# Optimization experiments

Hardware: AMD Instinct MI355X
Metric: run time of the kernel (lower is better)

The kernel has to match this reference:

```python
import jax, jax.numpy as jnp
import numpy as np

N, K, D_IN, D_OUT = 50000, 16, 256, 256
LN_EPS = 1e-5


def setup_inputs() -> dict:
    key = jax.random.key(0)
    k1, k2, k3, k4 = jax.random.split(key, 4)
    features = jax.random.normal(k1, (N, D_IN), dtype=jnp.float32)
    neighbors = jax.random.randint(k2, (N, K), 0, N, dtype=jnp.int64)
    importance_weights = jax.random.uniform(k3, (N, K), dtype=jnp.float32)
    # Linear(in_channels, out_channels): weight stored as [D_IN, D_OUT] for x @ W + b
    W = jax.random.normal(k4, (D_IN, D_OUT), dtype=jnp.float32) * (1.0 / np.sqrt(D_IN))
    b = jnp.zeros((D_OUT,), dtype=jnp.float32)
    gamma = jnp.ones((D_OUT,), dtype=jnp.float32)
    beta = jnp.zeros((D_OUT,), dtype=jnp.float32)
    return {"features": features, "neighbors": neighbors,
            "importance_weights": importance_weights,
            "W": W, "b": b, "gamma": gamma, "beta": beta}


def reference(features, neighbors, importance_weights, W, b, gamma, beta):
    # Gather neighbor features: [N, K, D_IN]
    neigh_feats = features[neighbors]
    # Linear transform: [N, K, D_OUT]
    transformed = jnp.einsum('nkd,df->nkf', neigh_feats, W) + b
    # Normalize importance weights per node; zero-sum fallback = uniform mean
    wsum = jnp.sum(importance_weights, axis=-1, keepdims=True)  # [N, 1]
    norm_w = jnp.where(wsum == 0.0,
                       jnp.full_like(importance_weights, 1.0 / K),
                       importance_weights / jnp.where(wsum == 0.0, 1.0, wsum))
    # Importance-weighted sum over neighbors: [N, D_OUT]
    agg = jnp.einsum('nkf,nk->nf', transformed, norm_w)
    # LayerNorm over feature dim (torch: biased variance, eps=1e-5)
    mean = jnp.mean(agg, axis=-1, keepdims=True)
    var = jnp.mean((agg - mean) ** 2, axis=-1, keepdims=True)
    out = (agg - mean) * jax.lax.rsqrt(var + LN_EPS) * gamma + beta
    return out
```

## Files before the change

kernel.cpp:

```cpp
#include <hip/hip_runtime.h>


#define NN   50000
#define KNB  16
#define D    256

typedef __attribute__((ext_vector_type(8))) short short8;
typedef __attribute__((ext_vector_type(4))) float f32x4;

static __device__ __forceinline__ unsigned short f2bf(float x) {
    unsigned int u = __float_as_uint(x);
    return (unsigned short)((u + 0x7FFFu + ((u >> 16) & 1u)) >> 16);
}
static __device__ __forceinline__ float bf2f(unsigned short h) {
    return __uint_as_float((unsigned int)h << 16);
}

__global__ __launch_bounds__(256) void convert_all(const float* __restrict__ feat,
                                                   const float* __restrict__ Wm,
                                                   unsigned short* __restrict__ featb,
                                                   unsigned short* __restrict__ wtp) {
    if (blockIdx.x < 6250) {
        const size_t g = (size_t)blockIdx.x * 256 + threadIdx.x;
        const float4 a = *(const float4*)(feat + g * 8);
        const float4 b = *(const float4*)(feat + g * 8 + 4);
        short8 o;
        o[0] = (short)f2bf(a.x); o[1] = (short)f2bf(a.y);
        o[2] = (short)f2bf(a.z); o[3] = (short)f2bf(a.w);
        o[4] = (short)f2bf(b.x); o[5] = (short)f2bf(b.y);
        o[6] = (short)f2bf(b.z); o[7] = (short)f2bf(b.w);
        *(short8*)(featb + g * 8) = o;
    } else {
        const int g    = (blockIdx.x - 6250) * 256 + threadIdx.x;
        const int lane = g & 63;
        const int kb   = (g >> 6) & 7;
        const int c    = g >> 9;
        const int n    = c * 16 + (lane & 15);
        const int k0   = kb * 32 + (lane >> 4) * 8;
        short8 v;
        #pragma unroll
        for (int j = 0; j < 8; ++j) v[j] = (short)f2bf(Wm[(size_t)(k0 + j) * D + n]);
        *(short8*)(wtp + (size_t)g * 8) = v;
    }
}

__global__ __launch_bounds__(256, 8) void pool_b(const unsigned short* __restrict__ featb,
                                                 const int*   __restrict__ nbr,
                                                 const float* __restrict__ iw,
                                                 unsigned short* __restrict__ aggb) {
    const int  t    = threadIdx.x;
    const int  lane = t & 63;
    const int  wq   = t >> 6;
    const long n    = (long)blockIdx.x * 4 + wq;

    float ws = 0.f;
    #pragma unroll
    for (int k = 0; k < KNB; ++k) ws += iw[n * KNB + k];
    const bool  zs  = (ws == 0.f);
    const float inv = zs ? (1.f / KNB) : (1.f / ws);

    float4 p = make_float4(0.f, 0.f, 0.f, 0.f);
    #pragma unroll 1
    for (int kb = 0; kb < KNB; kb += 8) {
        int   idx[8];
        float w[8];
        #pragma unroll
        for (int k = 0; k < 8; ++k) {
            idx[k] = nbr[n * KNB + kb + k];
            w[k]   = iw [n * KNB + kb + k];
        }
        #pragma unroll
        for (int k = 0; k < 8; ++k) {
            const float   wk = zs ? inv : (w[k] * inv);
            const ushort4 u  = *(const ushort4*)(featb + (size_t)idx[k] * D + lane * 4);
            p.x += wk * bf2f(u.x); p.y += wk * bf2f(u.y);
            p.z += wk * bf2f(u.z); p.w += wk * bf2f(u.w);
        }
    }
    ushort4 o;
    o.x = f2bf(p.x); o.y = f2bf(p.y); o.z = f2bf(p.z); o.w = f2bf(p.w);
    *(ushort4*)(aggb + (size_t)n * 512 + lane * 4) = o;
}

__global__ __launch_bounds__(256, 8) void pool_f(const float* __restrict__ feat,
                                                 const int*   __restrict__ nbr,
                                                 const float* __restrict__ iw,
                                                 unsigned short* __restrict__ aggb) {
    const int  t    = threadIdx.x;
    const int  lane = t & 63;
    const int  wq   = t >> 6;
    const long n    = (long)blockIdx.x * 4 + wq;
    float ws = 0.f;
    #pragma unroll
    for (int k = 0; k < KNB; ++k) ws += iw[n * KNB + k];
    const bool  zs  = (ws == 0.f);
    const float inv = zs ? (1.f / KNB) : (1.f / ws);
    float4 p = make_float4(0.f, 0.f, 0.f, 0.f);
    #pragma unroll 1
    for (int kb = 0; kb < KNB; kb += 8) {
        int idx[8]; float w[8];
        #pragma unroll
        for (int k = 0; k < 8; ++k) { idx[k] = nbr[n*KNB+kb+k]; w[k] = iw[n*KNB+kb+k]; }
        #pragma unroll
        for (int k = 0; k < 8; ++k) {
            const float  wk = zs ? inv : (w[k] * inv);
            const float4 f  = *(const float4*)(feat + (size_t)idx[k] * D + lane * 4);
            p.x += wk*f.x; p.y += wk*f.y; p.z += wk*f.z; p.w += wk*f.w;
        }
    }
    ushort4 o;
    o.x = f2bf(p.x); o.y = f2bf(p.y); o.z = f2bf(p.z); o.w = f2bf(p.w);
    *(ushort4*)(aggb + (size_t)n * 512 + lane * 4) = o;
}

#define WSTR 272
__global__ __launch_bounds__(256) void gemm_ln(const unsigned short* __restrict__ aggb,
                                               const unsigned short* __restrict__ wtp,
                                               const float* __restrict__ bias,
                                               const float* __restrict__ gamma,
                                               const float* __restrict__ beta,
                                               float* __restrict__ out) {
    __shared__ float fsh[4][4 * WSTR];

    const int t       = threadIdx.x;
    const int lane    = t & 63;
    const int wq      = t >> 6;
    const int quad    = lane >> 4;
    const int l15     = lane & 15;
    const int rowbase = blockIdx.x * 64 + wq * 16;

    const int arow = min(rowbase + l15, NN - 1);
    const unsigned short* aptr = aggb + (size_t)arow * 512 + quad * 8;
    const short8* wv = (const short8*)wtp;

    f32x4 acc[16];
    #pragma unroll
    for (int c = 0; c < 16; ++c) acc[c] = (f32x4){0.f, 0.f, 0.f, 0.f};

    #pragma unroll
    for (int kb = 0; kb < 8; ++kb) {
        const short8 a = *(const short8*)(aptr + kb * 32);
        #pragma unroll
        for (int c = 0; c < 16; ++c) {
            const short8 b = wv[(size_t)(c * 8 + kb) * 64 + lane];
            acc[c] = __builtin_amdgcn_mfma_f32_16x16x32_bf16(a, b, acc[c], 0, 0, 0);
        }
    }

    float bv[16];
    #pragma unroll
    for (int c = 0; c < 16; ++c) bv[c] = bias[c * 16 + l15];
    const float4 gv4 = *(const float4*)(gamma + lane * 4);
    const float4 bt4 = *(const float4*)(beta  + lane * 4);
    float* wsh = fsh[wq];

    #pragma unroll
    for (int j = 0; j < 4; ++j) {
        float s = 0.f, sq = 0.f;
        #pragma unroll
        for (int c = 0; c < 16; ++c) {
            const float v = acc[c][j] + bv[c];
            s += v; sq += v * v;
        }
        #pragma unroll
        for (int off = 1; off < 16; off <<= 1) {
            s  += __shfl_xor(s,  off, 64);
            sq += __shfl_xor(sq, off, 64);
        }
        const float mean = s * (1.f / D);
        const float var  = sq * (1.f / D) - mean * mean;
        const float rstd = rsqrtf(var + 1e-5f);
        #pragma unroll
        for (int c = 0; c < 16; ++c)
            wsh[quad * WSTR + c * 16 + l15] = (acc[c][j] + bv[c] - mean) * rstd;
        #pragma unroll
        for (int p = 0; p < 4; ++p) {
            const long  r  = rowbase + p * 4 + j;
            const float4 v = *(const float4*)(wsh + p * WSTR + lane * 4);
            float4 o;
            o.x = v.x * gv4.x + bt4.x; o.y = v.y * gv4.y + bt4.y;
            o.z = v.z * gv4.z + bt4.z; o.w = v.w * gv4.w + bt4.w;
            *(float4*)(out + r * D + lane * 4) = o;
        }
    }
}

extern "C" void kernel_launch(void* const* d_in, const int* in_sizes, int n_in,
                              void* d_out, int out_size, void* d_ws, size_t ws_size,
                              hipStream_t stream) {
    const float* feat = (const float*)d_in[0];
    const int*   nbr  = (const int*)d_in[1];
    const float* iw   = (const float*)d_in[2];
    const float* Wm   = (const float*)d_in[3];
    const float* b    = (const float*)d_in[4];
    const float* g    = (const float*)d_in[5];
    const float* be   = (const float*)d_in[6];
    float*       out  = (float*)d_out;

    unsigned short* wtp   = (unsigned short*)d_ws;
    unsigned short* featb = (unsigned short*)((char*)d_ws + 131072);
    unsigned short* aggb  = (unsigned short*)d_out;

    const size_t need = 131072 + (size_t)NN * D * 2;

    if (ws_size >= need) {
        convert_all<<<dim3(6282),    dim3(256), 0, stream>>>(feat, Wm, featb, wtp);
        pool_b     <<<dim3(NN / 4),  dim3(256), 0, stream>>>(featb, nbr, iw, aggb);
    } else {
        convert_all<<<dim3(32 + 6250), dim3(256), 0, stream>>>(feat, Wm, featb, wtp);
        pool_f     <<<dim3(NN / 4),  dim3(256), 0, stream>>>(feat, nbr, iw, aggb);
    }
    gemm_ln<<<dim3((NN + 63) / 64), dim3(256), 0, stream>>>(aggb, wtp, b, g, be, out);
}
```

Baseline: 188.0 us.

## Stage packed weight tiles in LDS with double buffering in GEMM+LayerNorm

The GEMM kernel now preloads all A fragments into registers and stages each 32-wide K slice of the packed bf16 weight matrix into shared memory. It double-buffers across K steps, so the four waves of a block share one global load of the weights instead of each wave reading them separately. The weight packing layout is reordered so that each K slice is contiguous, and the output store is guarded for the tail rows. The fallback path no longer runs feature conversion blocks it does not need. The cost is a block barrier per K step, 32KB of extra LDS per block, and added register pressure that may reduce occupancy.

```diff
diff --git a/kernel.cpp b/kernel.cpp
--- a/kernel.cpp
+++ b/kernel.cpp
@@ -4,6 +4,7 @@
 #define NN   50000
 #define KNB  16
 #define D    256
+#define WSTR 272
 
 typedef __attribute__((ext_vector_type(8))) short short8;
 typedef __attribute__((ext_vector_type(4))) float f32x4;
@@ -19,8 +20,9 @@
 __global__ __launch_bounds__(256) void convert_all(const float* __restrict__ feat,
                                                    const float* __restrict__ Wm,
                                                    unsigned short* __restrict__ featb,
-                                                   unsigned short* __restrict__ wtp) {
-    if (blockIdx.x < 6250) {
+                                                   unsigned short* __restrict__ wtp,
+                                                   int nfb) {
+    if ((int)blockIdx.x < nfb) {
         const size_t g = (size_t)blockIdx.x * 256 + threadIdx.x;
         const float4 a = *(const float4*)(feat + g * 8);
         const float4 b = *(const float4*)(feat + g * 8 + 4);
@@ -31,10 +33,10 @@
         o[6] = (short)f2bf(b.z); o[7] = (short)f2bf(b.w);
         *(short8*)(featb + g * 8) = o;
     } else {
-        const int g    = (blockIdx.x - 6250) * 256 + threadIdx.x;
+        const int g    = (blockIdx.x - nfb) * 256 + threadIdx.x;
         const int lane = g & 63;
-        const int kb   = (g >> 6) & 7;
-        const int c    = g >> 9;
+        const int c    = (g >> 6) & 15;
+        const int kb   = g >> 10;
         const int n    = c * 16 + (lane & 15);
         const int k0   = kb * 32 + (lane >> 4) * 8;
         short8 v;
@@ -113,13 +115,13 @@
     *(ushort4*)(aggb + (size_t)n * 512 + lane * 4) = o;
 }
 
-#define WSTR 272
 __global__ __launch_bounds__(256) void gemm_ln(const unsigned short* __restrict__ aggb,
                                                const unsigned short* __restrict__ wtp,
                                                const float* __restrict__ bias,
                                                const float* __restrict__ gamma,
                                                const float* __restrict__ beta,
                                                float* __restrict__ out) {
+    __shared__ short sB[2][8192];
     __shared__ float fsh[4][4 * WSTR];
 
     const int t       = threadIdx.x;
@@ -133,18 +135,39 @@
     const unsigned short* aptr = aggb + (size_t)arow * 512 + quad * 8;
     const short8* wv = (const short8*)wtp;
 
+    short8 aF[8];
+    #pragma unroll
+    for (int kb = 0; kb < 8; ++kb) aF[kb] = *(const short8*)(aptr + kb * 32);
+
+    #pragma unroll
+    for (int i = 0; i < 4; ++i)
+        *(short8*)&sB[0][(size_t)(i * 256 + t) * 8] = wv[i * 256 + t];
+    __syncthreads();
+
     f32x4 acc[16];
     #pragma unroll
     for (int c = 0; c < 16; ++c) acc[c] = (f32x4){0.f, 0.f, 0.f, 0.f};
 
     #pragma unroll
     for (int kb = 0; kb < 8; ++kb) {
-        const short8 a = *(const short8*)(aptr + kb * 32);
+        const int buf = kb & 1;
+        short8 stg[4];
+        if (kb < 7) {
+            #pragma unroll
+            for (int i = 0; i < 4; ++i)
+                stg[i] = wv[(size_t)(kb + 1) * 1024 + i * 256 + t];
+        }
         #pragma unroll
         for (int c = 0; c < 16; ++c) {
-            const short8 b = wv[(size_t)(c * 8 + kb) * 64 + lane];
-            acc[c] = __builtin_amdgcn_mfma_f32_16x16x32_bf16(a, b, acc[c], 0, 0, 0);
-        }
+            const short8 b = *(const short8*)&sB[buf][(size_t)(c * 64 + lane) * 8];
+            acc[c] = __builtin_amdgcn_mfma_f32_16x16x32_bf16(aF[kb], b, acc[c], 0, 0, 0);
+        }
+        if (kb < 7) {
+            #pragma unroll
+            for (int i = 0; i < 4; ++i)
+                *(short8*)&sB[buf ^ 1][(size_t)(i * 256 + t) * 8] = stg[i];
+        }
+        __syncthreads();
     }
 
     float bv[16];
@@ -176,11 +199,13 @@
         #pragma unroll
         for (int p = 0; p < 4; ++p) {
             const long  r  = rowbase + p * 4 + j;
-            const float4 v = *(const float4*)(wsh + p * WSTR + lane * 4);
-            float4 o;
-            o.x = v.x * gv4.x + bt4.x; o.y = v.y * gv4.y + bt4.y;
-            o.z = v.z * gv4.z + bt4.z; o.w = v.w * gv4.w + bt4.w;
-            *(float4*)(out + r * D + lane * 4) = o;
+            if (r < NN) {
+                const float4 v = *(const float4*)(wsh + p * WSTR + lane * 4);
+                float4 o;
+                o.x = v.x * gv4.x + bt4.x; o.y = v.y * gv4.y + bt4.y;
+                o.z = v.z * gv4.z + bt4.z; o.w = v.w * gv4.w + bt4.w;
+                *(float4*)(out + r * D + lane * 4) = o;
+            }
         }
     }
 }
@@ -204,11 +229,11 @@
     const size_t need = 131072 + (size_t)NN * D * 2;
 
     if (ws_size >= need) {
-        convert_all<<<dim3(6282),    dim3(256), 0, stream>>>(feat, Wm, featb, wtp);
-        pool_b     <<<dim3(NN / 4),  dim3(256), 0, stream>>>(featb, nbr, iw, aggb);
+        convert_all<<<dim3(6282),   dim3(256), 0, stream>>>(feat, Wm, featb, wtp, 6250);
+        pool_b     <<<dim3(NN / 4), dim3(256), 0, stream>>>(featb, nbr, iw, aggb);
     } else {
-        convert_all<<<dim3(32 + 6250), dim3(256), 0, stream>>>(feat, Wm, featb, wtp);
-        pool_f     <<<dim3(NN / 4),  dim3(256), 0, stream>>>(feat, nbr, iw, aggb);
+        convert_all<<<dim3(32),     dim3(256), 0, stream>>>(feat, Wm, featb, wtp, 0);
+        pool_f     <<<dim3(NN / 4), dim3(256), 0, stream>>>(feat, nbr, iw, aggb);
     }
     gemm_ln<<<dim3((NN + 63) / 64), dim3(256), 0, stream>>>(aggb, wtp, b, g, be, out);
 }
```

Measured after the change: 186.7 us. About the same (-0.6%).
